# Kernel optimization log

Hardware: AMD Instinct MI355X
Metric: run time of the kernel (lower is better)

## Reference

```python
import jax, jax.numpy as jnp
import numpy as np

QK_K = 256      # super-block size
N_SUB = 8       # sub-blocks per super-block
SUB_SIZE = QK_K // N_SUB  # 32
NMAX_4BIT = 15.0


def _quantize_scales_6bit(scales):
    # scales: (B, N_SUB). Quantize to 6-bit grid [0..63] and dequantize; STE for grads.
    s_min = scales.min(axis=-1, keepdims=True)
    s_max = scales.max(axis=-1, keepdims=True)
    s_range = jnp.maximum(s_max - s_min, 1e-8)
    s_int = jnp.clip(jnp.round((scales - s_min) / s_range * 63.0), 0.0, 63.0)
    s_dequant = s_int / 63.0 * s_range + s_min
    return scales + jax.lax.stop_gradient(s_dequant - scales)


def fake_quantize_q4_k_m(weight):
    orig_shape = weight.shape
    w = weight.reshape(-1)
    pad = (-w.size) % QK_K
    if pad:
        w = jnp.concatenate([w, jnp.zeros((pad,), dtype=w.dtype)])
    # (n_blocks, N_SUB, SUB_SIZE)
    w_sub = w.reshape(-1, N_SUB, SUB_SIZE)
    sub_min = jnp.minimum(w_sub.min(axis=-1), 0.0)   # clamp(max=0)
    sub_max = jnpum if False else jnp.maximum(w_sub.max(axis=-1), 0.0)  # clamp(min=0)
    scale_raw = jnp.maximum(sub_max - sub_min, 1e-8) / NMAX_4BIT
    scale = _quantize_scales_6bit(scale_raw)         # (n_blocks, N_SUB)
    # super-block min, rounded through fp16 with STE
    super_min_raw = sub_min.min(axis=-1, keepdims=True)  # (n_blocks, 1)
    super_min_f16 = super_min_raw.astype(jnp.float16).astype(w.dtype)
    super_min = super_min_raw + jax.lax.stop_gradient(super_min_f16 - super_min_raw)
    adj_min = sub_min - super_min                    # (n_blocks, N_SUB)
    scale_bc = jnp.maximum(scale, 1e-8)[..., None]   # (n_blocks, N_SUB, 1)
    w_int = (w_sub - super_min[..., None] - adj_min[..., None]) / scale_bc
    w_int = jnp.clip(jnp.round(w_int), 0.0, NMAX_4BIT)
    w_dequant = w_int * scale_bc + adj_min[..., None] + super_min[..., None]
    w_out = w_sub + jax.lax.stop_gradient(w_dequant - w_sub)  # STE
    w_flat = w_out.reshape(-1)
    if pad:
        w_flat = w_flat[:-pad]
    return w_flat.reshape(orig_shape)


def setup_inputs() -> dict:
    key = jax.random.key(0)
    k1, k2, k3 = jax.random.split(key, 3)
    x = jax.random.normal(k1, (2, 2048, 4096), dtype=jnp.float32)
    weight = jax.random.normal(k2, (4096, 4096), dtype=jnp.float32) * 0.02
    bias = jax.random.normal(k3, (4096,), dtype=jnp.float32)
    return {"x": x, "weight": weight, "bias": bias}


def reference(x, weight, bias):
    # _qmode = True path: fake-quantize weight to Q4_K_M grid, then dense linear.
    fq_weight = fake_quantize_q4_k_m(weight)
    return jnp.einsum('bsd,od->bso', x, fq_weight) + bias
```

## Files before the change

### kernel.cpp

```cpp
#include <hip/hip_runtime.h>
#include <hip/hip_bf16.h>
#include <hip/hip_fp16.h>


typedef __attribute__((ext_vector_type(8))) short bf16x8;
typedef __attribute__((ext_vector_type(8))) unsigned short ushort8;
typedef __attribute__((ext_vector_type(4))) float f32x4;

__device__ __forceinline__ unsigned short f2bf(float f) {
  unsigned int u = __float_as_uint(f);
  u += 0x7fffu + ((u >> 16) & 1u);
  return (unsigned short)(u >> 16);
}

__global__ __launch_bounds__(256) void prep_kernel(
    const float* __restrict__ x, unsigned short* __restrict__ xb,
    const float* __restrict__ w, unsigned short* __restrict__ wq,
    int castBlocks) {
  if ((int)blockIdx.x < castBlocks) {
    const size_t i = ((size_t)blockIdx.x * 256 + threadIdx.x) * 8;
    const float4 a = *(const float4*)(x + i);
    const float4 b = *(const float4*)(x + i + 4);
    ushort8 o = {f2bf(a.x), f2bf(a.y), f2bf(a.z), f2bf(a.w),
                 f2bf(b.x), f2bf(b.y), f2bf(b.z), f2bf(b.w)};
    *(ushort8*)(xb + i) = o;
    return;
  }
  const int qb   = blockIdx.x - castBlocks;
  const int lane = threadIdx.x & 63;
  const int wv   = threadIdx.x >> 6;
  const size_t base = (((size_t)qb * 4 + wv) * 256) + (size_t)lane * 4;
  const float4 v = *(const float4*)(w + base);

  float mn = fminf(fminf(v.x, v.y), fminf(v.z, v.w));
  float mx = fmaxf(fmaxf(v.x, v.y), fmaxf(v.z, v.w));
#pragma unroll
  for (int off = 1; off <= 4; off <<= 1) {
    mn = fminf(mn, __shfl_xor(mn, off));
    mx = fmaxf(mx, __shfl_xor(mx, off));
  }
  const float sub_min = fminf(mn, 0.0f);
  const float sub_max = fmaxf(mx, 0.0f);
  const float scale_raw = fmaxf(sub_max - sub_min, 1e-8f) / 15.0f;

  float smn = scale_raw, smx = scale_raw, supermin = sub_min;
#pragma unroll
  for (int off = 8; off <= 32; off <<= 1) {
    smn = fminf(smn, __shfl_xor(smn, off));
    smx = fmaxf(smx, __shfl_xor(smx, off));
    supermin = fminf(supermin, __shfl_xor(supermin, off));
  }
  const float s_range = fmaxf(smx - smn, 1e-8f);
  float s_int = rintf((scale_raw - smn) / s_range * 63.0f);
  s_int = fminf(fmaxf(s_int, 0.0f), 63.0f);
  float scale = s_int / 63.0f * s_range + smn;
  scale = fmaxf(scale, 1e-8f);
  const float inv_scale = 1.0f / scale;

  const float sm  = __half2float(__float2half(supermin));
  const float adj = sub_min - sm;

  float e[4] = {v.x, v.y, v.z, v.w};
  ushort4 o;
  unsigned short* op = (unsigned short*)&o;
#pragma unroll
  for (int k = 0; k < 4; ++k) {
    const float t = (e[k] - sm) - adj;
    float qv = rintf(t * inv_scale);
    qv = fminf(fmaxf(qv, 0.0f), 15.0f);
    op[k] = f2bf((qv * scale + adj) + sm);
  }
  *(ushort4*)(wq + base) = o;
}

#define BM 256
#define BN 128
#define BK 32

__device__ __forceinline__ void async_cp16(void* lds, const void* g) {
  __builtin_amdgcn_global_load_lds(
      (__attribute__((address_space(1))) void*)(void*)g,
      (__attribute__((address_space(3))) void*)lds, 16, 0, 0);
}

__global__ __launch_bounds__(256, 2) void gemm_bt_kernel(
    const unsigned short* __restrict__ A,
    const unsigned short* __restrict__ B,
    const float* __restrict__ bias,
    float* __restrict__ C,
    int M, int N, int K) {
  __shared__ unsigned short lds_a[2][BM * BK];
  __shared__ unsigned short lds_b[2][BN * BK];

  const int tid  = threadIdx.x;
  const int lane = tid & 63;
  const int wv   = tid >> 6;
  const int wm   = wv >> 1;
  const int wn   = wv & 1;
  const int bx   = blockIdx.x;
  const int by   = blockIdx.y;

  const int r0   = tid >> 2;
  const int cw   = (tid & 3) ^ ((tid >> 3) & 3);
  const int koff = cw * 8;

  const unsigned short* ga0 = A + (size_t)(by * BM + r0)       * K + koff;
  const unsigned short* ga1 = A + (size_t)(by * BM + r0 + 64)  * K + koff;
  const unsigned short* ga2 = A + (size_t)(by * BM + r0 + 128) * K + koff;
  const unsigned short* ga3 = A + (size_t)(by * BM + r0 + 192) * K + koff;
  const unsigned short* gb0 = B + (size_t)(bx * BN + r0)       * K + koff;
  const unsigned short* gb1 = B + (size_t)(bx * BN + r0 + 64)  * K + koff;

  const int lo0 = tid * 8, lo1 = (tid + 256) * 8,
            lo2 = (tid + 512) * 8, lo3 = (tid + 768) * 8;

  f32x4 acc[8][4] = {};

  const int arow  = wm * 128 + (lane & 15);
  const int brow  = wn * 64 + (lane & 15);
  const int kslot = (((lane >> 4) ^ ((lane >> 1) & 3))) * 8;

  async_cp16(lds_a[0] + lo0, ga0);
  async_cp16(lds_a[0] + lo1, ga1);
  async_cp16(lds_a[0] + lo2, ga2);
  async_cp16(lds_a[0] + lo3, ga3);
  async_cp16(lds_b[0] + lo0, gb0);
  async_cp16(lds_b[0] + lo1, gb1);

  for (int k0 = 0; k0 < K; k0 += BK) {
    const int cur = (k0 >> 5) & 1;
    __syncthreads();
    if (k0 + BK < K) {
      const int nxt = cur ^ 1;
      const int kn  = k0 + BK;
      async_cp16(lds_a[nxt] + lo0, ga0 + kn);
      async_cp16(lds_a[nxt] + lo1, ga1 + kn);
      async_cp16(lds_a[nxt] + lo2, ga2 + kn);
      async_cp16(lds_a[nxt] + lo3, ga3 + kn);
      async_cp16(lds_b[nxt] + lo0, gb0 + kn);
      async_cp16(lds_b[nxt] + lo1, gb1 + kn);
    }

    bf16x8 af[8], bfr[4];
#pragma unroll
    for (int i = 0; i < 8; ++i)
      af[i] = *(const bf16x8*)(lds_a[cur] + (arow + i * 16) * BK + kslot);
#pragma unroll
    for (int j = 0; j < 4; ++j)
      bfr[j] = *(const bf16x8*)(lds_b[cur] + (brow + j * 16) * BK + kslot);

#pragma unroll
    for (int i = 0; i < 8; ++i)
#pragma unroll
      for (int j = 0; j < 4; ++j)
        acc[i][j] = __builtin_amdgcn_mfma_f32_16x16x32_bf16(af[i], bfr[j],
                                                            acc[i][j], 0, 0, 0);
  }

  const int rbase = by * BM + wm * 128 + (lane >> 4) * 4;
  const int cbase = bx * BN + wn * 64 + (lane & 15);
#pragma unroll
  for (int j = 0; j < 4; ++j) {
    const int c = cbase + j * 16;
    const float bv = bias[c];
#pragma unroll
    for (int i = 0; i < 8; ++i) {
#pragma unroll
      for (int r = 0; r < 4; ++r) {
        C[(size_t)(rbase + i * 16 + r) * N + c] = acc[i][j][r] + bv;
      }
    }
  }
}

extern "C" void kernel_launch(void* const* d_in, const int* in_sizes, int n_in,
                              void* d_out, int out_size, void* d_ws, size_t ws_size,
                              hipStream_t stream) {
  const float* x    = (const float*)d_in[0];
  const float* w    = (const float*)d_in[1];
  const float* bias = (const float*)d_in[2];
  float* out = (float*)d_out;

  const long long xn = in_sizes[0];
  const long long wn = in_sizes[1];
  const int N = in_sizes[2];
  const int K = (int)(wn / N);
  const int M = (int)(xn / K);

  unsigned short* xb = (unsigned short*)d_ws;
  unsigned short* wb = xb + (size_t)M * K;

  const int castBlocks  = (int)(xn / (256 * 8));
  const int quantBlocks = (int)(wn / (256 * 4));
  prep_kernel<<<castBlocks + quantBlocks, 256, 0, stream>>>(x, xb, w, wb,
                                                            castBlocks);
  gemm_bt_kernel<<<dim3(N / BN, M / BM), 256, 0, stream>>>(xb, wb, bias, out,
                                                           M, N, K);
}
```

Measured before the change: 310.4 us.

## Use BK=64 single-buffered LDS tiles with a wider XOR swizzle in GEMM

Result: faster. 289.0 us (-6.9%).

```diff
diff --git a/kernel.cpp b/kernel.cpp
--- a/kernel.cpp
+++ b/kernel.cpp
@@ -75,7 +75,7 @@
 
 #define BM 256
 #define BN 128
-#define BK 32
+#define BK 64
 
 __device__ __forceinline__ void async_cp16(void* lds, const void* g) {
   __builtin_amdgcn_global_load_lds(
@@ -89,8 +89,8 @@
     const float* __restrict__ bias,
     float* __restrict__ C,
     int M, int N, int K) {
-  __shared__ unsigned short lds_a[2][BM * BK];
-  __shared__ unsigned short lds_b[2][BN * BK];
+  __shared__ unsigned short lds_a[BM * BK];
+  __shared__ unsigned short lds_b[BN * BK];
 
   const int tid  = threadIdx.x;
   const int lane = tid & 63;
@@ -100,61 +100,54 @@
   const int bx   = blockIdx.x;
   const int by   = blockIdx.y;
 
-  const int r0   = tid >> 2;
-  const int cw   = (tid & 3) ^ ((tid >> 3) & 3);
-  const int koff = cw * 8;
+  const int rloc = tid >> 3;
+  const int csw  = (tid & 7) ^ (rloc & 7);
+  const int koff = csw * 8;
 
-  const unsigned short* ga0 = A + (size_t)(by * BM + r0)       * K + koff;
-  const unsigned short* ga1 = A + (size_t)(by * BM + r0 + 64)  * K + koff;
-  const unsigned short* ga2 = A + (size_t)(by * BM + r0 + 128) * K + koff;
-  const unsigned short* ga3 = A + (size_t)(by * BM + r0 + 192) * K + koff;
-  const unsigned short* gb0 = B + (size_t)(bx * BN + r0)       * K + koff;
-  const unsigned short* gb1 = B + (size_t)(bx * BN + r0 + 64)  * K + koff;
-
-  const int lo0 = tid * 8, lo1 = (tid + 256) * 8,
-            lo2 = (tid + 512) * 8, lo3 = (tid + 768) * 8;
+  const unsigned short* gA[8];
+  const unsigned short* gB[4];
+#pragma unroll
+  for (int j = 0; j < 8; ++j)
+    gA[j] = A + (size_t)(by * BM + j * 32 + rloc) * K + koff;
+#pragma unroll
+  for (int j = 0; j < 4; ++j)
+    gB[j] = B + (size_t)(bx * BN + j * 32 + rloc) * K + koff;
 
   f32x4 acc[8][4] = {};
 
-  const int arow  = wm * 128 + (lane & 15);
-  const int brow  = wn * 64 + (lane & 15);
-  const int kslot = (((lane >> 4) ^ ((lane >> 1) & 3))) * 8;
-
-  async_cp16(lds_a[0] + lo0, ga0);
-  async_cp16(lds_a[0] + lo1, ga1);
-  async_cp16(lds_a[0] + lo2, ga2);
-  async_cp16(lds_a[0] + lo3, ga3);
-  async_cp16(lds_b[0] + lo0, gb0);
-  async_cp16(lds_b[0] + lo1, gb1);
+  const int arow   = wm * 128 + (lane & 15);
+  const int brow   = wn * 64 + (lane & 15);
+  const int kslot0 = (((lane >> 4) ^ (lane & 7))) * 8;
+  const int kslot1 = kslot0 ^ 32;
 
   for (int k0 = 0; k0 < K; k0 += BK) {
-    const int cur = (k0 >> 5) & 1;
-    __syncthreads();
-    if (k0 + BK < K) {
-      const int nxt = cur ^ 1;
-      const int kn  = k0 + BK;
-      async_cp16(lds_a[nxt] + lo0, ga0 + kn);
-      async_cp16(lds_a[nxt] + lo1, ga1 + kn);
-      async_cp16(lds_a[nxt] + lo2, ga2 + kn);
-      async_cp16(lds_a[nxt] + lo3, ga3 + kn);
-      async_cp16(lds_b[nxt] + lo0, gb0 + kn);
-      async_cp16(lds_b[nxt] + lo1, gb1 + kn);
-    }
-
-    bf16x8 af[8], bfr[4];
 #pragma unroll
-    for (int i = 0; i < 8; ++i)
-      af[i] = *(const bf16x8*)(lds_a[cur] + (arow + i * 16) * BK + kslot);
+    for (int j = 0; j < 8; ++j)
+      async_cp16(lds_a + j * 2048 + tid * 8, gA[j] + k0);
 #pragma unroll
     for (int j = 0; j < 4; ++j)
-      bfr[j] = *(const bf16x8*)(lds_b[cur] + (brow + j * 16) * BK + kslot);
+      async_cp16(lds_b + j * 2048 + tid * 8, gB[j] + k0);
+    __syncthreads();
 
 #pragma unroll
-    for (int i = 0; i < 8; ++i)
+    for (int h = 0; h < 2; ++h) {
+      const int ks = h ? kslot1 : kslot0;
+      bf16x8 af[8], bfr[4];
+#pragma unroll
+      for (int i = 0; i < 8; ++i)
+        af[i] = *(const bf16x8*)(lds_a + (arow + i * 16) * BK + ks);
 #pragma unroll
       for (int j = 0; j < 4; ++j)
-        acc[i][j] = __builtin_amdgcn_mfma_f32_16x16x32_bf16(af[i], bfr[j],
-                                                            acc[i][j], 0, 0, 0);
+        bfr[j] = *(const bf16x8*)(lds_b + (brow + j * 16) * BK + ks);
+
+#pragma unroll
+      for (int i = 0; i < 8; ++i)
+#pragma unroll
+        for (int j = 0; j < 4; ++j)
+          acc[i][j] = __builtin_amdgcn_mfma_f32_16x16x32_bf16(af[i], bfr[j],
+                                                              acc[i][j], 0, 0, 0);
+    }
+    __syncthreads();
   }
 
   const int rbase = by * BM + wm * 128 + (lane >> 4) * 4;
```
